# Kernel optimization log

Hardware: AMD Instinct MI355X
Metric: run time of the kernel (lower is better)

The kernel has to match this reference:

```python
import jax, jax.numpy as jnp
import numpy as np

N = 10000
K = 32
D_GROUP = 256  # per-group input features
OUT_DIM = 256


def setup_inputs() -> dict:
    key = jax.random.key(0)
    ks = jax.random.split(key, 6)
    x = jax.random.normal(ks[0], (N, 2 * D_GROUP), dtype=jnp.float32)
    W1 = jax.random.normal(ks[1], (OUT_DIM, D_GROUP), dtype=jnp.float32) / np.sqrt(D_GROUP)
    a1 = jax.random.uniform(ks[2], (OUT_DIM,), dtype=jnp.float32)
    W2 = jax.random.normal(ks[3], (OUT_DIM, D_GROUP), dtype=jnp.float32) / np.sqrt(D_GROUP)
    a2 = jax.random.uniform(ks[4], (OUT_DIM,), dtype=jnp.float32)
    graph = jax.random.randint(ks[5], (N, K), 0, N)  # precomputed kNN indices
    return {"x": x, "W1": W1, "a1": a1, "W2": W2, "a2": a2, "graph": graph}


def _gat_layer(xg, W, a, graph):
    # linear transform: (N, out_dim)
    out = xg @ W.T
    # rescale by softmax feature weights (gaussian kernel, rescale=True)
    fw = jax.nn.softmax(a)
    out = out * fw
    # nonlinearity_1 = Hardtanh
    out = jnp.clip(out, -1.0, 1.0)
    # gather k-NN features: (N, K, out_dim)
    neigh = out[graph]
    # gaussian attention score over neighbors: (N, K)
    att = -jnp.sum((out[:, None, :] - neigh) ** 2, axis=-1)
    att = jax.nn.softmax(att, axis=-1)
    # weighted neighbor aggregation: (N, out_dim)
    return jnp.einsum("nk,nkd->nd", att, neigh)


def reference(x, W1, a1, W2, a2, graph):
    y1 = _gat_layer(x[:, :D_GROUP], W1, a1, graph)
    y2 = _gat_layer(x[:, D_GROUP:], W2, a2, graph)
    # merge=False -> concatenate group outputs
    return jnp.concatenate([y1, y2], axis=-1)
```

## Files before the change

### kernel.cpp

```cpp
#include <hip/hip_runtime.h>
#include <math.h>

#define N_NODES 10000
#define K_NB    32
#define D       256
#define XD      512

typedef __attribute__((ext_vector_type(8))) short  short8;
typedef __attribute__((ext_vector_type(4))) float  f32x4;

__device__ __forceinline__ float clip1(float v) { return fminf(fmaxf(v, -1.f), 1.f); }

__device__ __forceinline__ unsigned int bf16_rne(float f) {
    unsigned int u = __float_as_uint(f);
    return (u + 0x7FFFu + ((u >> 16) & 1u)) >> 16;
}
__device__ __forceinline__ float bf16f(unsigned int h) { return __uint_as_float(h << 16); }
__device__ __forceinline__ float blo(unsigned int u) { return __uint_as_float(u << 16); }
__device__ __forceinline__ float bhif(unsigned int u) { return __uint_as_float(u & 0xFFFF0000u); }

__device__ __forceinline__ void cvt8(float4 A, float4 B, uint4& hi, uint4& lo) {
    const float v[8] = {A.x, A.y, A.z, A.w, B.x, B.y, B.z, B.w};
    unsigned int h[8], q[8];
    #pragma unroll
    for (int i = 0; i < 8; ++i) {
        h[i] = bf16_rne(v[i]);
        q[i] = bf16_rne(v[i] - bf16f(h[i]));
    }
    hi = make_uint4(h[0] | (h[1] << 16), h[2] | (h[3] << 16),
                    h[4] | (h[5] << 16), h[6] | (h[7] << 16));
    lo = make_uint4(q[0] | (q[1] << 16), q[2] | (q[3] << 16),
                    q[4] | (q[5] << 16), q[6] | (q[7] << 16));
}

__global__ __launch_bounds__(256)
void conv_w(const float* __restrict__ W1, const float* __restrict__ W2,
            unsigned short* __restrict__ Whi, unsigned short* __restrict__ Wlo)
{
    const int u    = blockIdx.x * 256 + threadIdx.x;
    const int gidx = u >> 13;
    const int rem  = u & 8191;
    const float* __restrict__ W = gidx ? W2 : W1;
    const float4 f0 = *(const float4*)&W[rem * 8];
    const float4 f1 = *(const float4*)&W[rem * 8 + 4];
    uint4 hi, lo;
    cvt8(f0, f1, hi, lo);
    *(uint4*)&Whi[gidx * 65536 + rem * 8] = hi;
    *(uint4*)&Wlo[gidx * 65536 + rem * 8] = lo;
}

__global__ __launch_bounds__(256, 4)
void gemm_mfma(const float* __restrict__ x,
               const float* __restrict__ a1, const float* __restrict__ a2,
               const unsigned short* __restrict__ Whi,
               const unsigned short* __restrict__ Wlo,
               unsigned short* __restrict__ t16)
{
    const int g = blockIdx.y;
    const float* __restrict__ a = g ? a2 : a1;
    const int slab = blockIdx.x;
    const int tid = threadIdx.x;
    const int w   = tid >> 6;
    const int l   = tid & 63;

    __shared__ float fwL[D];
    __shared__ float red[16];

    {
        float v = a[tid];
        float m = v;
        #pragma unroll
        for (int o = 32; o; o >>= 1) m = fmaxf(m, __shfl_xor(m, o));
        if ((tid & 63) == 0) red[tid >> 6] = m;
        __syncthreads();
        m = fmaxf(fmaxf(red[0], red[1]), fmaxf(red[2], red[3]));
        float e = expf(v - m);
        float s = e;
        #pragma unroll
        for (int o = 32; o; o >>= 1) s += __shfl_xor(s, o);
        if ((tid & 63) == 0) red[4 + (tid >> 6)] = s;
        __syncthreads();
        s = red[4] + red[5] + red[6] + red[7];
        fwL[tid] = e / s;
    }
    __syncthreads();

    const unsigned short* __restrict__ WhiG = Whi + (g << 16);
    const unsigned short* __restrict__ WloG = Wlo + (g << 16);

    f32x4 acc[4];
    #pragma unroll
    for (int i = 0; i < 4; ++i) acc[i] = (f32x4){0.f, 0.f, 0.f, 0.f};

    const int arow = slab * 16 + (l & 15);
    const int koff = 8 * (l >> 4);
    const int nt0  = w * 4;

    for (int kc = 0; kc < 8; ++kc) {
        const int kbase = kc * 32 + koff;
        const float* xp = &x[(size_t)arow * XD + g * D + kbase];
        const float4 xa = *(const float4*)&xp[0];
        const float4 xb = *(const float4*)&xp[4];
        uint4 ahi, alo;
        cvt8(xa, xb, ahi, alo);
        const short8 ah = __builtin_bit_cast(short8, ahi);
        const short8 al = __builtin_bit_cast(short8, alo);

        #pragma unroll
        for (int i = 0; i < 4; ++i) {
            const int brow = (nt0 + i) * 16 + (l & 15);
            const short8 bh = __builtin_bit_cast(short8, *(const uint4*)&WhiG[brow * 256 + kbase]);
            const short8 bl = __builtin_bit_cast(short8, *(const uint4*)&WloG[brow * 256 + kbase]);
            acc[i] = __builtin_amdgcn_mfma_f32_16x16x32_bf16(ah, bh, acc[i], 0, 0, 0);
            acc[i] = __builtin_amdgcn_mfma_f32_16x16x32_bf16(al, bh, acc[i], 0, 0, 0);
            acc[i] = __builtin_amdgcn_mfma_f32_16x16x32_bf16(ah, bl, acc[i], 0, 0, 0);
        }
    }

    #pragma unroll
    for (int i = 0; i < 4; ++i) {
        const int   col = (nt0 + i) * 16 + (l & 15);
        const float fw  = fwL[col];
        #pragma unroll
        for (int r = 0; r < 4; ++r) {
            const int row = slab * 16 + (l >> 4) * 4 + r;
            t16[(size_t)row * XD + g * D + col] =
                (unsigned short)bf16_rne(clip1(acc[i][r] * fw));
        }
    }
}

__global__ __launch_bounds__(256, 8)
void gat_aggregate(const unsigned short* __restrict__ t16,
                   const int* __restrict__ graph, float* __restrict__ out)
{
    const int n   = blockIdx.x;
    const int g   = blockIdx.y;
    const int tid = threadIdx.x;
    const int w   = tid >> 6;
    const int l   = tid & 63;

    __shared__ float part[4][D];
    __shared__ float Ssh[4];

    int rows[8];
    #pragma unroll
    for (int kk = 0; kk < 8; ++kk)
        rows[kk] = graph[(size_t)n * K_NB + (w + kk * 4)];

    const size_t gcol = (size_t)g * D + 4 * l;
    const uint2 ov = *(const uint2*)&t16[(size_t)n * XD + gcol];
    const float o0 = blo(ov.x), o1 = bhif(ov.x), o2 = blo(ov.y), o3 = bhif(ov.y);

    uint2 nbu[8];
    #pragma unroll
    for (int kk = 0; kk < 8; ++kk)
        nbu[kk] = *(const uint2*)&t16[(size_t)rows[kk] * XD + gcol];

    float nf[8][4];
    float d2p[8];
    #pragma unroll
    for (int kk = 0; kk < 8; ++kk) {
        nf[kk][0] = blo(nbu[kk].x); nf[kk][1] = bhif(nbu[kk].x);
        nf[kk][2] = blo(nbu[kk].y); nf[kk][3] = bhif(nbu[kk].y);
        const float dx = o0 - nf[kk][0], dy = o1 - nf[kk][1];
        const float dz = o2 - nf[kk][2], dw = o3 - nf[kk][3];
        d2p[kk] = dx * dx + dy * dy + dz * dz + dw * dw;
    }

    const bool b0 = l & 1, b1 = l & 2, b2 = l & 4;
    float u[4];
    #pragma unroll
    for (int i = 0; i < 4; ++i) {
        const float give = b0 ? d2p[2 * i] : d2p[2 * i + 1];
        const float keep = b0 ? d2p[2 * i + 1] : d2p[2 * i];
        u[i] = keep + __shfl_xor(give, 1);
    }
    float v[2];
    #pragma unroll
    for (int i = 0; i < 2; ++i) {
        const float give = b1 ? u[2 * i] : u[2 * i + 1];
        const float keep = b1 ? u[2 * i + 1] : u[2 * i];
        v[i] = keep + __shfl_xor(give, 2);
    }
    float d2 = (b2 ? v[1] : v[0]) + __shfl_xor(b2 ? v[0] : v[1], 4);
    d2 += __shfl_xor(d2, 8);
    d2 += __shfl_xor(d2, 16);
    d2 += __shfl_xor(d2, 32);

    const float e = __expf(-d2);

    float Sw = e;
    Sw += __shfl_xor(Sw, 1);
    Sw += __shfl_xor(Sw, 2);
    Sw += __shfl_xor(Sw, 4);

    const int base = l & 56;
    float4 p = make_float4(0.f, 0.f, 0.f, 0.f);
    #pragma unroll
    for (int kk = 0; kk < 8; ++kk) {
        const float ak = __shfl(e, base + kk);
        p.x += ak * nf[kk][0]; p.y += ak * nf[kk][1];
        p.z += ak * nf[kk][2]; p.w += ak * nf[kk][3];
    }

    *(float4*)&part[w][4 * l] = p;
    if (l == 0) Ssh[w] = Sw;
    __syncthreads();

    const float rS = 1.f / (Ssh[0] + Ssh[1] + Ssh[2] + Ssh[3]);
    const float y  = (part[0][tid] + part[1][tid] + part[2][tid] + part[3][tid]) * rS;
    out[(size_t)n * XD + (size_t)g * D + tid] = y;
}

extern "C" void kernel_launch(void* const* d_in, const int* in_sizes, int n_in,
                              void* d_out, int out_size, void* d_ws, size_t ws_size,
                              hipStream_t stream) {
    const float* x     = (const float*)d_in[0];
    const float* W1    = (const float*)d_in[1];
    const float* a1    = (const float*)d_in[2];
    const float* W2    = (const float*)d_in[3];
    const float* a2    = (const float*)d_in[4];
    const int*   graph = (const int*)d_in[5];
    float* out = (float*)d_out;

    unsigned short* t16 = (unsigned short*)d_ws;
    unsigned short* Whi = t16 + (size_t)N_NODES * XD;
    unsigned short* Wlo = Whi + 2 * 65536;

    conv_w<<<64, 256, 0, stream>>>(W1, W2, Whi, Wlo);

    dim3 grid1(N_NODES / 16, 2);
    gemm_mfma<<<grid1, 256, 0, stream>>>(x, a1, a2, Whi, Wlo, t16);

    dim3 grid2(N_NODES, 2);
    gat_aggregate<<<grid2, 256, 0, stream>>>(t16, graph, out);
}
```

Measured before the change: 154.7 us.

## Split GEMM output columns across two blocks and prefetch x row into registers

The GEMM grid gains a dimension that splits each 16-row slab's 256 output columns between two blocks, so each wave computes two 16-column tiles instead of four. All eight k-chunks of the x row are loaded into registers before the loop, which is fully unrolled, and the MFMAs of the two tiles are interleaved so independent accumulator chains alternate. Launch bounds are relaxed to 3 blocks per CU to allow more registers. The intent is more parallelism and better latency hiding in the GEMM. The cost is that each x row is loaded and converted to bf16 twice, and the fw softmax is recomputed in twice as many blocks.

```diff
diff --git a/kernel.cpp b/kernel.cpp
--- a/kernel.cpp
+++ b/kernel.cpp
@@ -49,16 +49,17 @@
     *(uint4*)&Wlo[gidx * 65536 + rem * 8] = lo;
 }
 
-__global__ __launch_bounds__(256, 4)
+__global__ __launch_bounds__(256, 3)
 void gemm_mfma(const float* __restrict__ x,
                const float* __restrict__ a1, const float* __restrict__ a2,
                const unsigned short* __restrict__ Whi,
                const unsigned short* __restrict__ Wlo,
                unsigned short* __restrict__ t16)
 {
-    const int g = blockIdx.y;
+    const int g = blockIdx.z;
     const float* __restrict__ a = g ? a2 : a1;
     const int slab = blockIdx.x;
+    const int cz   = blockIdx.y;
     const int tid = threadIdx.x;
     const int w   = tid >> 6;
     const int l   = tid & 63;
@@ -88,37 +89,51 @@
     const unsigned short* __restrict__ WhiG = Whi + (g << 16);
     const unsigned short* __restrict__ WloG = Wlo + (g << 16);
 
-    f32x4 acc[4];
-    #pragma unroll
-    for (int i = 0; i < 4; ++i) acc[i] = (f32x4){0.f, 0.f, 0.f, 0.f};
-
     const int arow = slab * 16 + (l & 15);
     const int koff = 8 * (l >> 4);
-    const int nt0  = w * 4;
-
+    const int nt0  = cz * 8 + w * 2;
+
+    float4 pxa[8], pxb[8];
+    const float* xrow = &x[(size_t)arow * XD + g * D + koff];
+    #pragma unroll
+    for (int kc = 0; kc < 8; ++kc) {
+        pxa[kc] = *(const float4*)&xrow[kc * 32];
+        pxb[kc] = *(const float4*)&xrow[kc * 32 + 4];
+    }
+
+    f32x4 acc[2];
+    acc[0] = (f32x4){0.f, 0.f, 0.f, 0.f};
+    acc[1] = (f32x4){0.f, 0.f, 0.f, 0.f};
+
+    #pragma unroll
     for (int kc = 0; kc < 8; ++kc) {
         const int kbase = kc * 32 + koff;
-        const float* xp = &x[(size_t)arow * XD + g * D + kbase];
-        const float4 xa = *(const float4*)&xp[0];
-        const float4 xb = *(const float4*)&xp[4];
         uint4 ahi, alo;
-        cvt8(xa, xb, ahi, alo);
+        cvt8(pxa[kc], pxb[kc], ahi, alo);
         const short8 ah = __builtin_bit_cast(short8, ahi);
         const short8 al = __builtin_bit_cast(short8, alo);
 
-        #pragma unroll
-        for (int i = 0; i < 4; ++i) {
-            const int brow = (nt0 + i) * 16 + (l & 15);
-            const short8 bh = __builtin_bit_cast(short8, *(const uint4*)&WhiG[brow * 256 + kbase]);
-            const short8 bl = __builtin_bit_cast(short8, *(const uint4*)&WloG[brow * 256 + kbase]);
-            acc[i] = __builtin_amdgcn_mfma_f32_16x16x32_bf16(ah, bh, acc[i], 0, 0, 0);
-            acc[i] = __builtin_amdgcn_mfma_f32_16x16x32_bf16(al, bh, acc[i], 0, 0, 0);
-            acc[i] = __builtin_amdgcn_mfma_f32_16x16x32_bf16(ah, bl, acc[i], 0, 0, 0);
-        }
-    }
-
-    #pragma unroll
-    for (int i = 0; i < 4; ++i) {
+        const int brow0 = (nt0 + 0) * 16 + (l & 15);
+        const int brow1 = (nt0 + 1) * 16 + (l & 15);
+        const uint4 bh0u = *(const uint4*)&WhiG[brow0 * 256 + kbase];
+        const uint4 bl0u = *(const uint4*)&WloG[brow0 * 256 + kbase];
+        const uint4 bh1u = *(const uint4*)&WhiG[brow1 * 256 + kbase];
+        const uint4 bl1u = *(const uint4*)&WloG[brow1 * 256 + kbase];
+        const short8 bh0 = __builtin_bit_cast(short8, bh0u);
+        const short8 bl0 = __builtin_bit_cast(short8, bl0u);
+        const short8 bh1 = __builtin_bit_cast(short8, bh1u);
+        const short8 bl1 = __builtin_bit_cast(short8, bl1u);
+
+        acc[0] = __builtin_amdgcn_mfma_f32_16x16x32_bf16(ah, bh0, acc[0], 0, 0, 0);
+        acc[1] = __builtin_amdgcn_mfma_f32_16x16x32_bf16(ah, bh1, acc[1], 0, 0, 0);
+        acc[0] = __builtin_amdgcn_mfma_f32_16x16x32_bf16(al, bh0, acc[0], 0, 0, 0);
+        acc[1] = __builtin_amdgcn_mfma_f32_16x16x32_bf16(al, bh1, acc[1], 0, 0, 0);
+        acc[0] = __builtin_amdgcn_mfma_f32_16x16x32_bf16(ah, bl0, acc[0], 0, 0, 0);
+        acc[1] = __builtin_amdgcn_mfma_f32_16x16x32_bf16(ah, bl1, acc[1], 0, 0, 0);
+    }
+
+    #pragma unroll
+    for (int i = 0; i < 2; ++i) {
         const int   col = (nt0 + i) * 16 + (l & 15);
         const float fw  = fwL[col];
         #pragma unroll
@@ -230,7 +245,7 @@
 
     conv_w<<<64, 256, 0, stream>>>(W1, W2, Whi, Wlo);
 
-    dim3 grid1(N_NODES / 16, 2);
+    dim3 grid1(N_NODES / 16, 2, 2);
     gemm_mfma<<<grid1, 256, 0, stream>>>(x, a1, a2, Whi, Wlo, t16);
 
     dim3 grid2(N_NODES, 2);
```

Result: slower. 162.5 us (+5.0%).

## Stage GEMM tiles in LDS via async global-to-LDS loads with swizzle

Applied to the files above, without the earlier changes.

The GEMM is retiled into 32-row by 128-column blocks, with an extra grid dimension splitting the output columns. Each k-chunk of x and of the hi/lo bf16 weights is staged into swizzled shared memory using global_load_lds, replacing the per-lane direct global loads. The aim is to cut redundant global traffic for the weights and get coalesced loads, at the cost of two barriers per k-step. The softmax of the feature weights is now recomputed by twice as many blocks, and a bounds check on rows is added.

```diff
diff --git a/kernel.cpp b/kernel.cpp
--- a/kernel.cpp
+++ b/kernel.cpp
@@ -8,6 +8,13 @@
 
 typedef __attribute__((ext_vector_type(8))) short  short8;
 typedef __attribute__((ext_vector_type(4))) float  f32x4;
+
+typedef __attribute__((address_space(1))) const unsigned int g_u32;
+typedef __attribute__((address_space(3))) unsigned int       l_u32;
+
+__device__ __forceinline__ void gld_lds16(const void* g, void* l) {
+    __builtin_amdgcn_global_load_lds((g_u32*)g, (l_u32*)l, 16, 0, 0);
+}
 
 __device__ __forceinline__ float clip1(float v) { return fminf(fmaxf(v, -1.f), 1.f); }
 
@@ -49,20 +56,24 @@
     *(uint4*)&Wlo[gidx * 65536 + rem * 8] = lo;
 }
 
-__global__ __launch_bounds__(256, 4)
+__global__ __launch_bounds__(256, 6)
 void gemm_mfma(const float* __restrict__ x,
                const float* __restrict__ a1, const float* __restrict__ a2,
                const unsigned short* __restrict__ Whi,
                const unsigned short* __restrict__ Wlo,
                unsigned short* __restrict__ t16)
 {
-    const int g = blockIdx.y;
+    const int slab = blockIdx.x;
+    const int cz   = blockIdx.y;
+    const int g    = blockIdx.z;
     const float* __restrict__ a = g ? a2 : a1;
-    const int slab = blockIdx.x;
     const int tid = threadIdx.x;
     const int w   = tid >> 6;
     const int l   = tid & 63;
 
+    __shared__ float          As[32 * 32];
+    __shared__ unsigned short Bhs[128 * 32];
+    __shared__ unsigned short Bls[128 * 32];
     __shared__ float fwL[D];
     __shared__ float red[16];
 
@@ -88,19 +99,43 @@
     const unsigned short* __restrict__ WhiG = Whi + (g << 16);
     const unsigned short* __restrict__ WloG = Wlo + (g << 16);
 
+    const int arloc = tid >> 3;
+    int agrow = slab * 32 + arloc;
+    if (agrow > N_NODES - 1) agrow = N_NODES - 1;
+    const int akg   = (tid & 7) ^ (arloc & 7);
+    const float* aSrcBase = &x[(size_t)agrow * XD + g * D + akg * 4];
+
+    const int brloc0 = tid >> 2;
+    const int brloc1 = brloc0 + 64;
+    const int bkg0   = (tid & 3) ^ ((brloc0 >> 1) & 3);
+    const int bkg1   = (tid & 3) ^ ((brloc1 >> 1) & 3);
+    const unsigned short* bhSrc0 = &WhiG[(cz * 128 + brloc0) * 256 + bkg0 * 8];
+    const unsigned short* bhSrc1 = &WhiG[(cz * 128 + brloc1) * 256 + bkg1 * 8];
+    const unsigned short* blSrc0 = &WloG[(cz * 128 + brloc0) * 256 + bkg0 * 8];
+    const unsigned short* blSrc1 = &WloG[(cz * 128 + brloc1) * 256 + bkg1 * 8];
+
+    const int woff = (tid >> 6) * 1024;
+
     f32x4 acc[4];
     #pragma unroll
     for (int i = 0; i < 4; ++i) acc[i] = (f32x4){0.f, 0.f, 0.f, 0.f};
 
-    const int arow = slab * 16 + (l & 15);
-    const int koff = 8 * (l >> 4);
-    const int nt0  = w * 4;
+    const int arow_l = 16 * (w >> 1) + (l & 15);
+    const int s      = l >> 4;
+    const int ct0    = (w & 1) * 4;
 
     for (int kc = 0; kc < 8; ++kc) {
-        const int kbase = kc * 32 + koff;
-        const float* xp = &x[(size_t)arow * XD + g * D + kbase];
-        const float4 xa = *(const float4*)&xp[0];
-        const float4 xb = *(const float4*)&xp[4];
+        gld_lds16(aSrcBase + kc * 32,  (char*)As  + woff);
+        gld_lds16(bhSrc0   + kc * 32,  (char*)Bhs + woff);
+        gld_lds16(bhSrc1   + kc * 32,  (char*)Bhs + 4096 + woff);
+        gld_lds16(blSrc0   + kc * 32,  (char*)Bls + woff);
+        gld_lds16(blSrc1   + kc * 32,  (char*)Bls + 4096 + woff);
+        __syncthreads();
+
+        const int kg0 = (2 * s)     ^ (arow_l & 7);
+        const int kg1 = (2 * s + 1) ^ (arow_l & 7);
+        const float4 xa = *(const float4*)((const char*)As + arow_l * 128 + kg0 * 16);
+        const float4 xb = *(const float4*)((const char*)As + arow_l * 128 + kg1 * 16);
         uint4 ahi, alo;
         cvt8(xa, xb, ahi, alo);
         const short8 ah = __builtin_bit_cast(short8, ahi);
@@ -108,24 +143,29 @@
 
         #pragma unroll
         for (int i = 0; i < 4; ++i) {
-            const int brow = (nt0 + i) * 16 + (l & 15);
-            const short8 bh = __builtin_bit_cast(short8, *(const uint4*)&WhiG[brow * 256 + kbase]);
-            const short8 bl = __builtin_bit_cast(short8, *(const uint4*)&WloG[brow * 256 + kbase]);
+            const int brow_l = (ct0 + i) * 16 + (l & 15);
+            const int bkg    = s ^ ((brow_l >> 1) & 3);
+            const short8 bh = __builtin_bit_cast(short8,
+                *(const uint4*)((const char*)Bhs + brow_l * 64 + bkg * 16));
+            const short8 bl = __builtin_bit_cast(short8,
+                *(const uint4*)((const char*)Bls + brow_l * 64 + bkg * 16));
             acc[i] = __builtin_amdgcn_mfma_f32_16x16x32_bf16(ah, bh, acc[i], 0, 0, 0);
             acc[i] = __builtin_amdgcn_mfma_f32_16x16x32_bf16(al, bh, acc[i], 0, 0, 0);
             acc[i] = __builtin_amdgcn_mfma_f32_16x16x32_bf16(ah, bl, acc[i], 0, 0, 0);
         }
+        __syncthreads();
     }
 
     #pragma unroll
     for (int i = 0; i < 4; ++i) {
-        const int   col = (nt0 + i) * 16 + (l & 15);
+        const int   col = cz * 128 + (ct0 + i) * 16 + (l & 15);
         const float fw  = fwL[col];
         #pragma unroll
         for (int r = 0; r < 4; ++r) {
-            const int row = slab * 16 + (l >> 4) * 4 + r;
-            t16[(size_t)row * XD + g * D + col] =
-                (unsigned short)bf16_rne(clip1(acc[i][r] * fw));
+            const int row = slab * 32 + 16 * (w >> 1) + (l >> 4) * 4 + r;
+            if (row < N_NODES)
+                t16[(size_t)row * XD + g * D + col] =
+                    (unsigned short)bf16_rne(clip1(acc[i][r] * fw));
         }
     }
 }
@@ -230,7 +270,7 @@
 
     conv_w<<<64, 256, 0, stream>>>(W1, W2, Whi, Wlo);
 
-    dim3 grid1(N_NODES / 16, 2);
+    dim3 grid1(313, 2, 2);
     gemm_mfma<<<grid1, 256, 0, stream>>>(x, a1, a2, Whi, Wlo, t16);
 
     dim3 grid2(N_NODES, 2);
```

Result: faster. 126.7 us (-18.1%).

## Stage x tile in LDS via async global_load_lds and retile GEMM to 32x128

Applied to the files above, without the earlier changes.

The GEMM kernel now loads a 32-row slab of x into swizzled shared memory using direct global-to-LDS loads, and each block computes a 32x128 output tile split across a new grid dimension. Before, each block handled 16 rows and all 256 columns, reading x straight from global memory. The aim is better reuse of the x and W fragments across waves and coalesced async loading of x. In exchange it uses 32KB of LDS per block, which may cut occupancy, and it adds boundary clamping for the partial last slab.

```diff
diff --git a/kernel.cpp b/kernel.cpp
--- a/kernel.cpp
+++ b/kernel.cpp
@@ -8,6 +8,13 @@
 
 typedef __attribute__((ext_vector_type(8))) short  short8;
 typedef __attribute__((ext_vector_type(4))) float  f32x4;
+
+typedef __attribute__((address_space(1))) const unsigned int g_u32;
+typedef __attribute__((address_space(3))) unsigned int       l_u32;
+
+__device__ __forceinline__ void gld_lds16(const void* g, void* l) {
+    __builtin_amdgcn_global_load_lds((g_u32*)g, (l_u32*)l, 16, 0, 0);
+}
 
 __device__ __forceinline__ float clip1(float v) { return fminf(fmaxf(v, -1.f), 1.f); }
 
@@ -56,15 +63,30 @@
                const unsigned short* __restrict__ Wlo,
                unsigned short* __restrict__ t16)
 {
-    const int g = blockIdx.y;
+    const int slab = blockIdx.x;
+    const int cz   = blockIdx.y;
+    const int g    = blockIdx.z;
     const float* __restrict__ a = g ? a2 : a1;
-    const int slab = blockIdx.x;
     const int tid = threadIdx.x;
     const int w   = tid >> 6;
     const int l   = tid & 63;
 
+    __shared__ float As[32 * 256];
     __shared__ float fwL[D];
     __shared__ float red[16];
+
+    {
+        const int row  = (w & 3);
+        #pragma unroll
+        for (int j = 0; j < 8; ++j) {
+            const int rloc = j * 4 + row;
+            int grow = slab * 32 + rloc;
+            if (grow > N_NODES - 1) grow = N_NODES - 1;
+            const int sg = l ^ (rloc & 7);
+            gld_lds16(&x[(size_t)grow * XD + g * D + sg * 4],
+                      (char*)As + j * 4096 + w * 1024);
+        }
+    }
 
     {
         float v = a[tid];
@@ -92,15 +114,19 @@
     #pragma unroll
     for (int i = 0; i < 4; ++i) acc[i] = (f32x4){0.f, 0.f, 0.f, 0.f};
 
-    const int arow = slab * 16 + (l & 15);
-    const int koff = 8 * (l >> 4);
-    const int nt0  = w * 4;
-
+    const int arow_l = 16 * (w >> 1) + (l & 15);
+    const int s      = l >> 4;
+    const int ct0    = (w & 1) * 4;
+    const char* Arow = (const char*)As + arow_l * 1024;
+    const int   rz   = arow_l & 7;
+
+    #pragma unroll
     for (int kc = 0; kc < 8; ++kc) {
-        const int kbase = kc * 32 + koff;
-        const float* xp = &x[(size_t)arow * XD + g * D + kbase];
-        const float4 xa = *(const float4*)&xp[0];
-        const float4 xb = *(const float4*)&xp[4];
+        const int kbase = kc * 32 + 8 * s;
+        const int g0 = (kc * 8 + 2 * s)     ^ rz;
+        const int g1 = (kc * 8 + 2 * s + 1) ^ rz;
+        const float4 xa = *(const float4*)(Arow + g0 * 16);
+        const float4 xb = *(const float4*)(Arow + g1 * 16);
         uint4 ahi, alo;
         cvt8(xa, xb, ahi, alo);
         const short8 ah = __builtin_bit_cast(short8, ahi);
@@ -108,9 +134,11 @@
 
         #pragma unroll
         for (int i = 0; i < 4; ++i) {
-            const int brow = (nt0 + i) * 16 + (l & 15);
-            const short8 bh = __builtin_bit_cast(short8, *(const uint4*)&WhiG[brow * 256 + kbase]);
-            const short8 bl = __builtin_bit_cast(short8, *(const uint4*)&WloG[brow * 256 + kbase]);
+            const int brow = cz * 128 + (ct0 + i) * 16 + (l & 15);
+            const short8 bh = __builtin_bit_cast(short8,
+                *(const uint4*)&WhiG[brow * 256 + kbase]);
+            const short8 bl = __builtin_bit_cast(short8,
+                *(const uint4*)&WloG[brow * 256 + kbase]);
             acc[i] = __builtin_amdgcn_mfma_f32_16x16x32_bf16(ah, bh, acc[i], 0, 0, 0);
             acc[i] = __builtin_amdgcn_mfma_f32_16x16x32_bf16(al, bh, acc[i], 0, 0, 0);
             acc[i] = __builtin_amdgcn_mfma_f32_16x16x32_bf16(ah, bl, acc[i], 0, 0, 0);
@@ -119,13 +147,14 @@
 
     #pragma unroll
     for (int i = 0; i < 4; ++i) {
-        const int   col = (nt0 + i) * 16 + (l & 15);
+        const int   col = cz * 128 + (ct0 + i) * 16 + (l & 15);
         const float fw  = fwL[col];
         #pragma unroll
         for (int r = 0; r < 4; ++r) {
-            const int row = slab * 16 + (l >> 4) * 4 + r;
-            t16[(size_t)row * XD + g * D + col] =
-                (unsigned short)bf16_rne(clip1(acc[i][r] * fw));
+            const int row = slab * 32 + 16 * (w >> 1) + (l >> 4) * 4 + r;
+            if (row < N_NODES)
+                t16[(size_t)row * XD + g * D + col] =
+                    (unsigned short)bf16_rne(clip1(acc[i][r] * fw));
         }
     }
 }
@@ -230,7 +259,7 @@
 
     conv_w<<<64, 256, 0, stream>>>(W1, W2, Whi, Wlo);
 
-    dim3 grid1(N_NODES / 16, 2);
+    dim3 grid1(313, 2, 2);
     gemm_mfma<<<grid1, 256, 0, stream>>>(x, a1, a2, Whi, Wlo, t16);
 
     dim3 grid2(N_NODES, 2);
```

Measured after the change: 158.6 us. +2.5%, slower.
